# Performance work log

Measured on AMD Instinct MI355X. Metric: run time of the kernel, lower is better.

Reference implementation:

```python
import jax, jax.numpy as jnp
import numpy as np

N = 100000      # entity nodes
E = 1000000     # edges per relation
D_IN = 256
HID = 128
EPS = 1e-16     # PyG softmax denominator eps
NEG_SLOPE = 0.2 # GATConv default leaky_relu slope


def _gat_conv(x, ei, Ws, Wd, a_s, a_d, b):
    """Single-head GATConv (heads=1, concat=False) with self-loops."""
    n = x.shape[0]
    loop = jnp.arange(n, dtype=ei.dtype)
    src = jnp.concatenate([ei[0], loop])  # [E+N]
    dst = jnp.concatenate([ei[1], loop])
    h_src = x @ Ws                         # [N, HID]
    h_dst = x @ Wd                         # [N, HID]
    a_src = h_src @ a_s                    # [N]
    a_dst = h_dst @ a_d                    # [N]
    e = jax.nn.leaky_relu(a_src[src] + a_dst[dst], NEG_SLOPE)  # [E+N]
    # numerically-stable softmax over incoming edges of each dst node
    m = jax.ops.segment_max(e, dst, num_segments=n)
    ex = jnp.exp(e - m[dst])
    denom = jax.ops.segment_sum(ex, dst, num_segments=n)
    alpha = ex / (denom[dst] + EPS)        # [E+N]
    out = jax.ops.segment_sum(alpha[:, None] * h_src[src], dst, num_segments=n)
    return out + b


def setup_inputs() -> dict:
    key = jax.random.key(0)
    ks = jax.random.split(key, 9)
    s_in = 1.0 / np.sqrt(D_IN)
    s_h = 1.0 / np.sqrt(HID)
    return {
        "x": jax.random.normal(ks[0], (N, D_IN), dtype=jnp.float32),
        "edge_index_r0": jax.random.randint(ks[1], (2, E), 0, N, dtype=jnp.int64)
                         if jax.config.jax_enable_x64 else jax.random.randint(ks[1], (2, E), 0, N).astype(jnp.int32),
        "edge_index_r1": jax.random.randint(ks[2], (2, E), 0, N, dtype=jnp.int64)
                         if jax.config.jax_enable_x64 else jax.random.randint(ks[2], (2, E), 0, N).astype(jnp.int32),
        "W_src": jax.random.normal(ks[3], (2, D_IN, HID), dtype=jnp.float32) * s_in,
        "W_dst": jax.random.normal(ks[4], (2, D_IN, HID), dtype=jnp.float32) * s_in,
        "att_src": jax.random.normal(ks[5], (2, HID), dtype=jnp.float32) * s_h,
        "att_dst": jax.random.normal(ks[6], (2, HID), dtype=jnp.float32) * s_h,
        "bias": jnp.zeros((2, HID), dtype=jnp.float32),
    }


def reference(x, edge_index_r0, edge_index_r1, W_src, W_dst, att_src, att_dst, bias):
    # HeteroConv aggr='sum' over the two entity->entity relations
    out = _gat_conv(x, edge_index_r0, W_src[0], W_dst[0], att_src[0], att_dst[0], bias[0])
    out = out + _gat_conv(x, edge_index_r1, W_src[1], W_dst[1], att_src[1], att_dst[1], bias[1])
    # ELU; dropout p=0.0 is identity
    return jax.nn.elu(out)
```

## Files before the change

kernel.cpp:

```cpp
#include <hip/hip_runtime.h>

typedef __attribute__((ext_vector_type(8))) __bf16 bf16x8;
typedef __attribute__((ext_vector_type(4))) float floatx4;

__device__ __forceinline__ float bf2f(unsigned short u) {
    return __uint_as_float(((unsigned)u) << 16);
}
__device__ __forceinline__ unsigned short f2bf(float f) {
    unsigned u = __float_as_uint(f);
    unsigned r = u + 0x7FFFu + ((u >> 16) & 1u);
    return (unsigned short)(r >> 16);
}

__global__ void detect_k(const unsigned short* __restrict__ xs, int* __restrict__ flag) {
    __shared__ int sred[256];
    int tid = threadIdx.x;
    int cnt = 0;
    for (int j = 0; j < 16; ++j) {
        unsigned short u = xs[(tid * 16 + j) * 2];
        int e = (u >> 7) & 0xFF;
        cnt += (e >= 96 && e <= 159) ? 1 : 0;
    }
    sred[tid] = cnt;
    __syncthreads();
    for (int s = 128; s > 0; s >>= 1) {
        if (tid < s) sred[tid] += sred[tid + s];
        __syncthreads();
    }
    if (tid == 0) *flag = (sred[0] > 2048) ? 1 : 0;
}

__device__ __forceinline__ void canon8(const void* src, unsigned short* dst,
                                       long long idx, int f) {
    if (f) {
        *(uint4*)&dst[idx] = *(const uint4*)((const unsigned short*)src + idx);
    } else {
        const float* sf = (const float*)src;
        unsigned short v[8];
        for (int j = 0; j < 8; ++j) v[j] = f2bf(sf[idx + j]);
        *(uint4*)&dst[idx] = *(const uint4*)v;
    }
}

__global__ void canon5_k(const void* Ws, const void* Wd, const void* as,
                         const void* ad, const void* b,
                         unsigned short* Wsb, unsigned short* Wdb,
                         unsigned short* asb, unsigned short* adb,
                         unsigned short* bsb, const int* __restrict__ flag) {
    int blk = blockIdx.x, tid = threadIdx.x;
    int f = *flag;
    if (blk < 64) {
        const void* src = blk < 32 ? Ws : Wd;
        unsigned short* dst = blk < 32 ? Wsb : Wdb;
        long long idx = ((long long)(blk & 31) * 256 + tid) * 8;
        canon8(src, dst, idx, f);
    } else {
        if (tid < 32)       canon8(as, asb, (long long)tid * 8, f);
        else if (tid < 64)  canon8(ad, adb, (long long)(tid - 32) * 8, f);
        else if (tid < 96)  canon8(b,  bsb, (long long)(tid - 64) * 8, f);
    }
}

__global__ void vec_kernel(const unsigned short* __restrict__ Ws,
                           const unsigned short* __restrict__ Wd,
                           const unsigned short* __restrict__ as_,
                           const unsigned short* __restrict__ ad_,
                           float* __restrict__ vecs) {
    int r = blockIdx.x;
    int k = threadIdx.x;
    float s = 0.f, t = 0.f;
    const unsigned short* wsrow = Ws + (size_t)r * 32768 + (size_t)k * 128;
    const unsigned short* wdrow = Wd + (size_t)r * 32768 + (size_t)k * 128;
    for (int h = 0; h < 128; ++h) {
        s += bf2f(wsrow[h]) * bf2f(as_[r * 128 + h]);
        t += bf2f(wdrow[h]) * bf2f(ad_[r * 128 + h]);
    }
    vecs[(r * 2 + 0) * 256 + k] = s;
    vecs[(r * 2 + 1) * 256 + k] = t;
}

__global__ void transpose_W(const unsigned short* __restrict__ W,
                            unsigned short* __restrict__ Bt) {
    int i = blockIdx.x * 256 + threadIdx.x;
    if (i >= 2 * 256 * 128) return;
    int r = i >> 15, rem = i & 32767;
    int k = rem >> 7, n = rem & 127;
    Bt[(size_t)r * 32768 + n * 256 + k] = W[i];
}

__global__ __launch_bounds__(256) void a_canon_k(const void* __restrict__ xraw,
                                                 unsigned short* __restrict__ xb,
                                                 const float* __restrict__ vecs,
                                                 float* __restrict__ aout, int n,
                                                 const int* __restrict__ flag) {
    __shared__ float sv[1024];
    int tid = threadIdx.x;
    for (int j = 0; j < 4; ++j) sv[j * 256 + tid] = vecs[j * 256 + tid];
    __syncthreads();
    int lane = tid & 63, wave = tid >> 6;
    int row = blockIdx.x * 4 + wave;
    if (row >= n) return;
    float xf[4];
    if (*flag) {
        uint2 u = *(const uint2*)((const unsigned short*)xraw + (size_t)row * 256 + lane * 4);
        xf[0] = bf2f((unsigned short)(u.x & 0xFFFF));
        xf[1] = bf2f((unsigned short)(u.x >> 16));
        xf[2] = bf2f((unsigned short)(u.y & 0xFFFF));
        xf[3] = bf2f((unsigned short)(u.y >> 16));
        *(uint2*)&xb[(size_t)row * 256 + lane * 4] = u;
    } else {
        float4 f = *(const float4*)((const float*)xraw + (size_t)row * 256 + lane * 4);
        xf[0] = f.x; xf[1] = f.y; xf[2] = f.z; xf[3] = f.w;
        unsigned short v[4] = {f2bf(f.x), f2bf(f.y), f2bf(f.z), f2bf(f.w)};
        *(uint2*)&xb[(size_t)row * 256 + lane * 4] = *(const uint2*)v;
    }
    float s[4] = {0.f, 0.f, 0.f, 0.f};
    for (int j = 0; j < 4; ++j)
        for (int q = 0; q < 4; ++q)
            s[j] += xf[q] * sv[j * 256 + lane * 4 + q];
    for (int j = 0; j < 4; ++j)
        for (int off = 32; off > 0; off >>= 1)
            s[j] += __shfl_down(s[j], off);
    if (lane == 0)
        for (int j = 0; j < 4; ++j) aout[(size_t)j * n + row] = s[j];
}

__global__ __launch_bounds__(256) void gemm_h(const unsigned short* __restrict__ x,
                                              const unsigned short* __restrict__ Btg,
                                              unsigned short* __restrict__ hout, int n) {
    const int r = blockIdx.y;
    const unsigned short* bt = Btg + (size_t)r * 32768;
    unsigned short* h = hout + (size_t)r * n * 128;
    const int r0 = blockIdx.x * 128;
    __shared__ __align__(16) unsigned short As[128 * 40];
    __shared__ __align__(16) unsigned short Bs[128 * 40];
    int tid = threadIdx.x;
    int lane = tid & 63, wave = tid >> 6;

    floatx4 acc[2][8];
    for (int mt = 0; mt < 2; ++mt)
        for (int nt = 0; nt < 8; ++nt)
            acc[mt][nt] = (floatx4){0.f, 0.f, 0.f, 0.f};

    for (int k0 = 0; k0 < 256; k0 += 32) {
        for (int i = 0; i < 2; ++i) {
            int L = i * 256 + tid;
            int row = L >> 2, kc = (L & 3) * 8;
            uint4 va = make_uint4(0u, 0u, 0u, 0u);
            int gr = r0 + row;
            if (gr < n) va = *(const uint4*)&x[(size_t)gr * 256 + k0 + kc];
            *(uint4*)&As[row * 40 + kc] = va;
            uint4 vb = *(const uint4*)&bt[(size_t)row * 256 + k0 + kc];
            *(uint4*)&Bs[row * 40 + kc] = vb;
        }
        __syncthreads();
        int qk = (lane >> 4) * 8;
        int m16 = lane & 15;
        bf16x8 af[2], bfv[8];
        af[0] = *(const bf16x8*)&As[(wave * 32 + m16) * 40 + qk];
        af[1] = *(const bf16x8*)&As[(wave * 32 + 16 + m16) * 40 + qk];
        for (int nt = 0; nt < 8; ++nt)
            bfv[nt] = *(const bf16x8*)&Bs[(nt * 16 + m16) * 40 + qk];
        for (int mt = 0; mt < 2; ++mt)
            for (int nt = 0; nt < 8; ++nt)
                acc[mt][nt] = __builtin_amdgcn_mfma_f32_16x16x32_bf16(
                    af[mt], bfv[nt], acc[mt][nt], 0, 0, 0);
        __syncthreads();
    }
    int col0 = lane & 15;
    for (int mt = 0; mt < 2; ++mt) {
        int baser = r0 + wave * 32 + mt * 16 + (lane >> 4) * 4;
        for (int nt = 0; nt < 8; ++nt)
            for (int i = 0; i < 4; ++i) {
                int gr = baser + i;
                if (gr < n) h[(size_t)gr * 128 + nt * 16 + col0] = f2bf(acc[mt][nt][i]);
            }
    }
}

__global__ void hist2_k(const int* __restrict__ ei0, const int* __restrict__ ei1,
                        int* __restrict__ cnt0, int* __restrict__ cnt1,
                        int* __restrict__ rank0, int* __restrict__ rank1,
                        int E_, int n) {
    int rel = blockIdx.y;
    const int* ei = rel ? ei1 : ei0;
    int* cnt = rel ? cnt1 : cnt0;
    int* rank = rel ? rank1 : rank0;
    int t = blockIdx.x * 256 + threadIdx.x;
    if (t >= E_ + n) return;
    int d = (t < E_) ? ei[E_ + t] : (t - E_);
    rank[t] = atomicAdd(&cnt[d], 1);
}

__global__ __launch_bounds__(256) void scan_red_k(const int* __restrict__ cnt0,
                                                  const int* __restrict__ cnt1,
                                                  int* __restrict__ part,
                                                  int n, int nb) {
    __shared__ int s[256];
    int rel = blockIdx.y;
    const int* cnt = rel ? cnt1 : cnt0;
    int i = blockIdx.x * 256 + threadIdx.x;
    s[threadIdx.x] = (i < n) ? cnt[i] : 0;
    __syncthreads();
    for (int o = 128; o > 0; o >>= 1) {
        if (threadIdx.x < o) s[threadIdx.x] += s[threadIdx.x + o];
        __syncthreads();
    }
    if (threadIdx.x == 0) part[rel * nb + blockIdx.x] = s[0];
}

__global__ __launch_bounds__(1024) void scan_mid_k(int* __restrict__ part, int nb) {
    __shared__ int s[1024];
    int rel = blockIdx.x;
    int t = threadIdx.x;
    s[t] = (t < nb) ? part[rel * nb + t] : 0;
    __syncthreads();
    for (int o = 1; o < 1024; o <<= 1) {
        int v = (t >= o) ? s[t - o] : 0;
        __syncthreads();
        s[t] += v;
        __syncthreads();
    }
    if (t < nb) part[rel * nb + t] = (t == 0) ? 0 : s[t - 1];
}

__global__ __launch_bounds__(256) void scan_off_k(const int* __restrict__ cnt0,
                                                  const int* __restrict__ cnt1,
                                                  const int* __restrict__ part,
                                                  int* __restrict__ off0,
                                                  int* __restrict__ off1,
                                                  int n, int nb) {
    __shared__ int s[256];
    int rel = blockIdx.y;
    const int* cnt = rel ? cnt1 : cnt0;
    int* off = rel ? off1 : off0;
    int i = blockIdx.x * 256 + threadIdx.x;
    int t = threadIdx.x;
    int v = (i < n) ? cnt[i] : 0;
    s[t] = v;
    __syncthreads();
    for (int o = 1; o < 256; o <<= 1) {
        int u = (t >= o) ? s[t - o] : 0;
        __syncthreads();
        s[t] += u;
        __syncthreads();
    }
    if (i < n) off[i] = part[rel * nb + blockIdx.x] + s[t] - v;
}

__global__ void fill2_k(const int* __restrict__ ei0, const int* __restrict__ ei1,
                        const float* __restrict__ avals,
                        const int* __restrict__ off0, const int* __restrict__ off1,
                        const int* __restrict__ rank0, const int* __restrict__ rank1,
                        unsigned long long* __restrict__ pair0,
                        unsigned long long* __restrict__ pair1,
                        int E_, int n) {
    int rel = blockIdx.y;
    const int* ei = rel ? ei1 : ei0;
    const float* as_ = avals + (rel ? 2 * (size_t)n : 0);
    const float* ad_ = avals + (rel ? 3 * (size_t)n : (size_t)n);
    const int* off = rel ? off1 : off0;
    const int* rank = rel ? rank1 : rank0;
    unsigned long long* pair = rel ? pair1 : pair0;
    int t = blockIdx.x * 256 + threadIdx.x;
    if (t >= E_ + n) return;
    int s, d;
    if (t < E_) { s = ei[t]; d = ei[E_ + t]; } else { s = t - E_; d = s; }
    float e = as_[s] + ad_[d];
    e = e > 0.f ? e : 0.2f * e;
    int pos = off[d] + rank[t];
    pair[pos] = ((unsigned long long)__float_as_uint(e) << 32) | (unsigned)s;
}

__device__ __forceinline__ void acc8(float* a, float w, const uint4& hv) {
    a[0] += w * bf2f((unsigned short)(hv.x & 0xFFFFu));
    a[1] += w * bf2f((unsigned short)(hv.x >> 16));
    a[2] += w * bf2f((unsigned short)(hv.y & 0xFFFFu));
    a[3] += w * bf2f((unsigned short)(hv.y >> 16));
    a[4] += w * bf2f((unsigned short)(hv.z & 0xFFFFu));
    a[5] += w * bf2f((unsigned short)(hv.z >> 16));
    a[6] += w * bf2f((unsigned short)(hv.w & 0xFFFFu));
    a[7] += w * bf2f((unsigned short)(hv.w >> 16));
}

__device__ __forceinline__ void rel_acc4(int d, int g, int l, int lane,
                                         const int* __restrict__ off,
                                         const int* __restrict__ cnt,
                                         const unsigned long long* __restrict__ pair,
                                         const unsigned short* __restrict__ h,
                                         float* __restrict__ o ) {
    int s0 = off[d];
    int e0 = s0 + cnt[d];
    float m = -1e30f;
    for (int i = s0 + lane; i < e0; i += 64)
        m = fmaxf(m, __uint_as_float((unsigned)(pair[i] >> 32)));
    for (int o_ = 1; o_ < 64; o_ <<= 1) m = fmaxf(m, __shfl_xor(m, o_));
    float denom = 0.f;
    float a[8] = {0.f, 0.f, 0.f, 0.f, 0.f, 0.f, 0.f, 0.f};
    int last = e0 - 1;
    for (int base = s0; base < e0; base += 8) {
        int i0 = base + g, i1 = i0 + 4;
        int j0 = min(i0, last), j1 = min(i1, last);
        unsigned long long p0 = pair[j0];
        unsigned long long p1 = pair[j1];
        int sA = (int)(unsigned)p0;
        int sB = (int)(unsigned)p1;
        uint4 hv0 = *(const uint4*)&h[(size_t)sA * 128 + l * 8];
        uint4 hv1 = *(const uint4*)&h[(size_t)sB * 128 + l * 8];
        float w0 = __expf(__uint_as_float((unsigned)(p0 >> 32)) - m);
        float w1 = __expf(__uint_as_float((unsigned)(p1 >> 32)) - m);
        w0 = (i0 < e0) ? w0 : 0.f;
        w1 = (i1 < e0) ? w1 : 0.f;
        denom += w0 + w1;
        acc8(a, w0, hv0);
        acc8(a, w1, hv1);
    }
    for (int j = 0; j < 8; ++j) {
        a[j] += __shfl_xor(a[j], 16);
        a[j] += __shfl_xor(a[j], 32);
    }
    denom += __shfl_xor(denom, 16);
    denom += __shfl_xor(denom, 32);
    float inv = 1.f / (denom + 1e-16f);
    for (int j = 0; j < 8; ++j) o[j] = a[j] * inv;
}

__global__ __launch_bounds__(256) void agg_k(
    const int* __restrict__ off0, const int* __restrict__ cnt0,
    const unsigned long long* __restrict__ pair0,
    const int* __restrict__ off1, const int* __restrict__ cnt1,
    const unsigned long long* __restrict__ pair1,
    const unsigned short* __restrict__ h0, const unsigned short* __restrict__ h1,
    const unsigned short* __restrict__ bias, void* __restrict__ out,
    int n, const int* __restrict__ flag) {
    int wave = threadIdx.x >> 6, lane = threadIdx.x & 63;
    int g = lane >> 4, l = lane & 15;
    int d = blockIdx.x * 4 + wave;
    if (d >= n) return;
    float p[8], q[8];
    rel_acc4(d, g, l, lane, off0, cnt0, pair0, h0, p);
    rel_acc4(d, g, l, lane, off1, cnt1, pair1, h1, q);
    uint4 b0 = *(const uint4*)&bias[l * 8];
    uint4 b1 = *(const uint4*)&bias[128 + l * 8];
    const unsigned* b0u = (const unsigned*)&b0;
    const unsigned* b1u = (const unsigned*)&b1;
    float v[8];
    for (int j = 0; j < 8; ++j) {
        unsigned w0 = b0u[j >> 1], w1 = b1u[j >> 1];
        float bb = bf2f((unsigned short)((j & 1) ? (w0 >> 16) : (w0 & 0xFFFFu)))
                 + bf2f((unsigned short)((j & 1) ? (w1 >> 16) : (w1 & 0xFFFFu)));
        float t = p[j] + q[j] + bb;
        v[j] = t > 0.f ? t : (__expf(t) - 1.f);
    }
    if (g == 0) {
        if (*flag) {
            unsigned pk[4];
            for (int j = 0; j < 4; ++j)
                pk[j] = ((unsigned)f2bf(v[2 * j + 1]) << 16) | (unsigned)f2bf(v[2 * j]);
            ((uint4*)out)[(size_t)d * 16 + l] = *(const uint4*)pk;
        } else {
            float4 f0 = make_float4(v[0], v[1], v[2], v[3]);
            float4 f1 = make_float4(v[4], v[5], v[6], v[7]);
            ((float4*)out)[(size_t)d * 32 + l * 2] = f0;
            ((float4*)out)[(size_t)d * 32 + l * 2 + 1] = f1;
        }
    }
}

static inline char* carve(char*& p, size_t bytes) {
    char* r = p;
    p += (bytes + 255) & ~(size_t)255;
    return r;
}

extern "C" void kernel_launch(void* const* d_in, const int* in_sizes, int n_in,
                              void* d_out, int out_size, void* d_ws, size_t ws_size,
                              hipStream_t stream) {
    (void)n_in; (void)out_size; (void)ws_size;
    const void* x_raw  = d_in[0];
    const int*  ei0    = (const int*)d_in[1];
    const int*  ei1    = (const int*)d_in[2];
    const void* Ws_raw = d_in[3];
    const void* Wd_raw = d_in[4];
    const void* as_raw = d_in[5];
    const void* ad_raw = d_in[6];
    const void* b_raw  = d_in[7];

    const int n = in_sizes[0] / 256;
    const int e = in_sizes[1] / 2;
    const int tot = e + n;
    const int nb = (n + 255) / 256;

    char* p = (char*)d_ws;
    float* avals = (float*)carve(p, (size_t)4 * n * 4);
    int*   cnt0  = (int*)carve(p, (size_t)2 * n * 4);
    int*   cnt1  = cnt0 + n;
    int*   off0  = (int*)carve(p, (size_t)n * 4);
    int*   off1  = (int*)carve(p, (size_t)n * 4);
    int*   part  = (int*)carve(p, (size_t)2 * nb * 4);
    int*   rank0 = (int*)carve(p, (size_t)tot * 4);
    int*   rank1 = (int*)carve(p, (size_t)tot * 4);
    unsigned long long* pair0 = (unsigned long long*)carve(p, (size_t)tot * 8);
    unsigned long long* pair1 = (unsigned long long*)carve(p, (size_t)tot * 8);
    float* vecs  = (float*)carve(p, 1024 * 4);
    int*   flag  = (int*)carve(p, 256);
    unsigned short* xb  = (unsigned short*)carve(p, (size_t)n * 256 * 2);
    unsigned short* h0  = (unsigned short*)carve(p, (size_t)2 * n * 128 * 2);
    unsigned short* h1  = h0 + (size_t)n * 128;
    unsigned short* Wsb = (unsigned short*)carve(p, 65536 * 2);
    unsigned short* Wdb = (unsigned short*)carve(p, 65536 * 2);
    unsigned short* Bt  = (unsigned short*)carve(p, 65536 * 2);
    unsigned short* asb = (unsigned short*)carve(p, 256 * 2);
    unsigned short* adb = (unsigned short*)carve(p, 256 * 2);
    unsigned short* bsb = (unsigned short*)carve(p, 256 * 2);

    hipMemsetAsync(cnt0, 0, (size_t)2 * n * 4, stream);

    detect_k<<<1, 256, 0, stream>>>((const unsigned short*)x_raw, flag);
    canon5_k<<<65, 256, 0, stream>>>(Ws_raw, Wd_raw, as_raw, ad_raw, b_raw,
                                     Wsb, Wdb, asb, adb, bsb, flag);
    vec_kernel<<<2, 256, 0, stream>>>(Wsb, Wdb, asb, adb, vecs);
    transpose_W<<<(2 * 256 * 128 + 255) / 256, 256, 0, stream>>>(Wsb, Bt);

    int gb = (tot + 255) / 256;
    hist2_k<<<dim3(gb, 2), 256, 0, stream>>>(ei0, ei1, cnt0, cnt1, rank0, rank1, e, n);
    scan_red_k<<<dim3(nb, 2), 256, 0, stream>>>(cnt0, cnt1, part, n, nb);
    scan_mid_k<<<2, 1024, 0, stream>>>(part, nb);
    scan_off_k<<<dim3(nb, 2), 256, 0, stream>>>(cnt0, cnt1, part, off0, off1, n, nb);

    a_canon_k<<<(n + 3) / 4, 256, 0, stream>>>(x_raw, xb, vecs, avals, n, flag);
    gemm_h<<<dim3((n + 127) / 128, 2), 256, 0, stream>>>(xb, Bt, h0, n);

    fill2_k<<<dim3(gb, 2), 256, 0, stream>>>(ei0, ei1, avals, off0, off1,
                                             rank0, rank1, pair0, pair1, e, n);

    agg_k<<<(n + 3) / 4, 256, 0, stream>>>(off0, cnt0, pair0, off1, cnt1, pair1,
                                           h0, h1, bsb, d_out, n, flag);
}
```

Before: 500.6 us.

## Fuse input canonicalization into consumers and drop segment-max pass in aggregation

```diff
diff --git a/kernel.cpp b/kernel.cpp
--- a/kernel.cpp
+++ b/kernel.cpp
@@ -2,6 +2,7 @@
 
 typedef __attribute__((ext_vector_type(8))) __bf16 bf16x8;
 typedef __attribute__((ext_vector_type(4))) float floatx4;
+typedef unsigned long long ull;
 
 __device__ __forceinline__ float bf2f(unsigned short u) {
     return __uint_as_float(((unsigned)u) << 16);
@@ -30,69 +31,41 @@
     if (tid == 0) *flag = (sred[0] > 2048) ? 1 : 0;
 }
 
-__device__ __forceinline__ void canon8(const void* src, unsigned short* dst,
-                                       long long idx, int f) {
-    if (f) {
-        *(uint4*)&dst[idx] = *(const uint4*)((const unsigned short*)src + idx);
-    } else {
-        const float* sf = (const float*)src;
-        unsigned short v[8];
-        for (int j = 0; j < 8; ++j) v[j] = f2bf(sf[idx + j]);
-        *(uint4*)&dst[idx] = *(const uint4*)v;
-    }
-}
-
-__global__ void canon5_k(const void* Ws, const void* Wd, const void* as,
-                         const void* ad, const void* b,
-                         unsigned short* Wsb, unsigned short* Wdb,
-                         unsigned short* asb, unsigned short* adb,
-                         unsigned short* bsb, const int* __restrict__ flag) {
-    int blk = blockIdx.x, tid = threadIdx.x;
-    int f = *flag;
-    if (blk < 64) {
-        const void* src = blk < 32 ? Ws : Wd;
-        unsigned short* dst = blk < 32 ? Wsb : Wdb;
-        long long idx = ((long long)(blk & 31) * 256 + tid) * 8;
-        canon8(src, dst, idx, f);
-    } else {
-        if (tid < 32)       canon8(as, asb, (long long)tid * 8, f);
-        else if (tid < 64)  canon8(ad, adb, (long long)(tid - 32) * 8, f);
-        else if (tid < 96)  canon8(b,  bsb, (long long)(tid - 64) * 8, f);
-    }
-}
-
-__global__ void vec_kernel(const unsigned short* __restrict__ Ws,
-                           const unsigned short* __restrict__ Wd,
-                           const unsigned short* __restrict__ as_,
-                           const unsigned short* __restrict__ ad_,
-                           float* __restrict__ vecs) {
+__device__ __forceinline__ float getf(const void* p, size_t i, int f) {
+    return f ? bf2f(((const unsigned short*)p)[i]) : ((const float*)p)[i];
+}
+
+__global__ void vec_kernel(const void* __restrict__ Ws, const void* __restrict__ Wd,
+                           const void* __restrict__ as_, const void* __restrict__ ad_,
+                           float* __restrict__ vecs, const int* __restrict__ flag) {
     int r = blockIdx.x;
     int k = threadIdx.x;
+    int f = *flag;
     float s = 0.f, t = 0.f;
-    const unsigned short* wsrow = Ws + (size_t)r * 32768 + (size_t)k * 128;
-    const unsigned short* wdrow = Wd + (size_t)r * 32768 + (size_t)k * 128;
+    size_t wbase = (size_t)r * 32768 + (size_t)k * 128;
     for (int h = 0; h < 128; ++h) {
-        s += bf2f(wsrow[h]) * bf2f(as_[r * 128 + h]);
-        t += bf2f(wdrow[h]) * bf2f(ad_[r * 128 + h]);
+        s += getf(Ws, wbase + h, f) * getf(as_, r * 128 + h, f);
+        t += getf(Wd, wbase + h, f) * getf(ad_, r * 128 + h, f);
     }
     vecs[(r * 2 + 0) * 256 + k] = s;
     vecs[(r * 2 + 1) * 256 + k] = t;
 }
 
-__global__ void transpose_W(const unsigned short* __restrict__ W,
-                            unsigned short* __restrict__ Bt) {
+__global__ void transpose_W(const void* __restrict__ W, unsigned short* __restrict__ Bt,
+                            const int* __restrict__ flag) {
     int i = blockIdx.x * 256 + threadIdx.x;
     if (i >= 2 * 256 * 128) return;
+    int f = *flag;
+    unsigned short v = f ? ((const unsigned short*)W)[i] : f2bf(((const float*)W)[i]);
     int r = i >> 15, rem = i & 32767;
-    int k = rem >> 7, n = rem & 127;
-    Bt[(size_t)r * 32768 + n * 256 + k] = W[i];
-}
-
-__global__ __launch_bounds__(256) void a_canon_k(const void* __restrict__ xraw,
-                                                 unsigned short* __restrict__ xb,
-                                                 const float* __restrict__ vecs,
-                                                 float* __restrict__ aout, int n,
-                                                 const int* __restrict__ flag) {
+    int k = rem >> 7, nn = rem & 127;
+    Bt[(size_t)r * 32768 + nn * 256 + k] = v;
+}
+
+__global__ __launch_bounds__(256) void a_k(const void* __restrict__ xraw,
+                                           const float* __restrict__ vecs,
+                                           float* __restrict__ aout, int n,
+                                           const int* __restrict__ flag) {
     __shared__ float sv[1024];
     int tid = threadIdx.x;
     for (int j = 0; j < 4; ++j) sv[j * 256 + tid] = vecs[j * 256 + tid];
@@ -107,12 +80,9 @@
         xf[1] = bf2f((unsigned short)(u.x >> 16));
         xf[2] = bf2f((unsigned short)(u.y & 0xFFFF));
         xf[3] = bf2f((unsigned short)(u.y >> 16));
-        *(uint2*)&xb[(size_t)row * 256 + lane * 4] = u;
     } else {
         float4 f = *(const float4*)((const float*)xraw + (size_t)row * 256 + lane * 4);
         xf[0] = f.x; xf[1] = f.y; xf[2] = f.z; xf[3] = f.w;
-        unsigned short v[4] = {f2bf(f.x), f2bf(f.y), f2bf(f.z), f2bf(f.w)};
-        *(uint2*)&xb[(size_t)row * 256 + lane * 4] = *(const uint2*)v;
     }
     float s[4] = {0.f, 0.f, 0.f, 0.f};
     for (int j = 0; j < 4; ++j)
@@ -125,13 +95,15 @@
         for (int j = 0; j < 4; ++j) aout[(size_t)j * n + row] = s[j];
 }
 
-__global__ __launch_bounds__(256) void gemm_h(const unsigned short* __restrict__ x,
+__global__ __launch_bounds__(256) void gemm_h(const void* __restrict__ xraw,
                                               const unsigned short* __restrict__ Btg,
-                                              unsigned short* __restrict__ hout, int n) {
+                                              unsigned short* __restrict__ hout, int n,
+                                              const int* __restrict__ flag) {
     const int r = blockIdx.y;
     const unsigned short* bt = Btg + (size_t)r * 32768;
     unsigned short* h = hout + (size_t)r * n * 128;
     const int r0 = blockIdx.x * 128;
+    const int fl = *flag;
     __shared__ __align__(16) unsigned short As[128 * 40];
     __shared__ __align__(16) unsigned short Bs[128 * 40];
     int tid = threadIdx.x;
@@ -148,7 +120,18 @@
             int row = L >> 2, kc = (L & 3) * 8;
             uint4 va = make_uint4(0u, 0u, 0u, 0u);
             int gr = r0 + row;
-            if (gr < n) va = *(const uint4*)&x[(size_t)gr * 256 + k0 + kc];
+            if (gr < n) {
+                if (fl) {
+                    va = *(const uint4*)((const unsigned short*)xraw + (size_t)gr * 256 + k0 + kc);
+                } else {
+                    const float* xf = (const float*)xraw + (size_t)gr * 256 + k0 + kc;
+                    float4 f0 = *(const float4*)xf;
+                    float4 f1 = *(const float4*)(xf + 4);
+                    unsigned short v[8] = {f2bf(f0.x), f2bf(f0.y), f2bf(f0.z), f2bf(f0.w),
+                                           f2bf(f1.x), f2bf(f1.y), f2bf(f1.z), f2bf(f1.w)};
+                    va = *(const uint4*)v;
+                }
+            }
             *(uint4*)&As[row * 40 + kc] = va;
             uint4 vb = *(const uint4*)&bt[(size_t)row * 256 + k0 + kc];
             *(uint4*)&Bs[row * 40 + kc] = vb;
@@ -252,8 +235,7 @@
                         const float* __restrict__ avals,
                         const int* __restrict__ off0, const int* __restrict__ off1,
                         const int* __restrict__ rank0, const int* __restrict__ rank1,
-                        unsigned long long* __restrict__ pair0,
-                        unsigned long long* __restrict__ pair1,
+                        ull* __restrict__ pair0, ull* __restrict__ pair1,
                         int E_, int n) {
     int rel = blockIdx.y;
     const int* ei = rel ? ei1 : ei0;
@@ -261,99 +243,103 @@
     const float* ad_ = avals + (rel ? 3 * (size_t)n : (size_t)n);
     const int* off = rel ? off1 : off0;
     const int* rank = rel ? rank1 : rank0;
-    unsigned long long* pair = rel ? pair1 : pair0;
+    ull* pair = rel ? pair1 : pair0;
     int t = blockIdx.x * 256 + threadIdx.x;
     if (t >= E_ + n) return;
     int s, d;
     if (t < E_) { s = ei[t]; d = ei[E_ + t]; } else { s = t - E_; d = s; }
     float e = as_[s] + ad_[d];
     e = e > 0.f ? e : 0.2f * e;
+    float w = __expf(e);
     int pos = off[d] + rank[t];
-    pair[pos] = ((unsigned long long)__float_as_uint(e) << 32) | (unsigned)s;
-}
-
-__device__ __forceinline__ void acc8(float* a, float w, const uint4& hv) {
-    a[0] += w * bf2f((unsigned short)(hv.x & 0xFFFFu));
-    a[1] += w * bf2f((unsigned short)(hv.x >> 16));
-    a[2] += w * bf2f((unsigned short)(hv.y & 0xFFFFu));
-    a[3] += w * bf2f((unsigned short)(hv.y >> 16));
-    a[4] += w * bf2f((unsigned short)(hv.z & 0xFFFFu));
-    a[5] += w * bf2f((unsigned short)(hv.z >> 16));
-    a[6] += w * bf2f((unsigned short)(hv.w & 0xFFFFu));
-    a[7] += w * bf2f((unsigned short)(hv.w >> 16));
-}
-
-__device__ __forceinline__ void rel_acc4(int d, int g, int l, int lane,
+    pair[pos] = ((ull)__float_as_uint(w) << 32) | (unsigned)s;
+}
+
+__device__ __forceinline__ void accw(float2* a, float w, const uint4& hv) {
+    const unsigned* u = (const unsigned*)&hv;
+    for (int j = 0; j < 4; ++j) {
+        float lo = __uint_as_float(u[j] << 16);
+        float hi = __uint_as_float(u[j] & 0xFFFF0000u);
+        a[j].x += w * lo;
+        a[j].y += w * hi;
+    }
+}
+
+__device__ __forceinline__ void rel_accS(int d, int g, int l,
                                          const int* __restrict__ off,
                                          const int* __restrict__ cnt,
-                                         const unsigned long long* __restrict__ pair,
+                                         const ull* __restrict__ pair,
                                          const unsigned short* __restrict__ h,
-                                         float* __restrict__ o ) {
+                                         float2* __restrict__ o ) {
     int s0 = off[d];
     int e0 = s0 + cnt[d];
-    float m = -1e30f;
-    for (int i = s0 + lane; i < e0; i += 64)
-        m = fmaxf(m, __uint_as_float((unsigned)(pair[i] >> 32)));
-    for (int o_ = 1; o_ < 64; o_ <<= 1) m = fmaxf(m, __shfl_xor(m, o_));
     float denom = 0.f;
-    float a[8] = {0.f, 0.f, 0.f, 0.f, 0.f, 0.f, 0.f, 0.f};
+    float2 a[4] = {{0.f, 0.f}, {0.f, 0.f}, {0.f, 0.f}, {0.f, 0.f}};
     int last = e0 - 1;
     for (int base = s0; base < e0; base += 8) {
         int i0 = base + g, i1 = i0 + 4;
         int j0 = min(i0, last), j1 = min(i1, last);
-        unsigned long long p0 = pair[j0];
-        unsigned long long p1 = pair[j1];
+        ull p0 = pair[j0];
+        ull p1 = pair[j1];
         int sA = (int)(unsigned)p0;
         int sB = (int)(unsigned)p1;
         uint4 hv0 = *(const uint4*)&h[(size_t)sA * 128 + l * 8];
         uint4 hv1 = *(const uint4*)&h[(size_t)sB * 128 + l * 8];
-        float w0 = __expf(__uint_as_float((unsigned)(p0 >> 32)) - m);
-        float w1 = __expf(__uint_as_float((unsigned)(p1 >> 32)) - m);
+        float w0 = __uint_as_float((unsigned)(p0 >> 32));
+        float w1 = __uint_as_float((unsigned)(p1 >> 32));
         w0 = (i0 < e0) ? w0 : 0.f;
         w1 = (i1 < e0) ? w1 : 0.f;
         denom += w0 + w1;
-        acc8(a, w0, hv0);
-        acc8(a, w1, hv1);
-    }
-    for (int j = 0; j < 8; ++j) {
-        a[j] += __shfl_xor(a[j], 16);
-        a[j] += __shfl_xor(a[j], 32);
+        accw(a, w0, hv0);
+        accw(a, w1, hv1);
+    }
+    for (int j = 0; j < 4; ++j) {
+        a[j].x += __shfl_xor(a[j].x, 16);
+        a[j].x += __shfl_xor(a[j].x, 32);
+        a[j].y += __shfl_xor(a[j].y, 16);
+        a[j].y += __shfl_xor(a[j].y, 32);
     }
     denom += __shfl_xor(denom, 16);
     denom += __shfl_xor(denom, 32);
     float inv = 1.f / (denom + 1e-16f);
-    for (int j = 0; j < 8; ++j) o[j] = a[j] * inv;
+    for (int j = 0; j < 4; ++j) { o[j].x = a[j].x * inv; o[j].y = a[j].y * inv; }
 }
 
 __global__ __launch_bounds__(256) void agg_k(
     const int* __restrict__ off0, const int* __restrict__ cnt0,
-    const unsigned long long* __restrict__ pair0,
+    const ull* __restrict__ pair0,
     const int* __restrict__ off1, const int* __restrict__ cnt1,
-    const unsigned long long* __restrict__ pair1,
+    const ull* __restrict__ pair1,
     const unsigned short* __restrict__ h0, const unsigned short* __restrict__ h1,
-    const unsigned short* __restrict__ bias, void* __restrict__ out,
+    const void* __restrict__ bias_raw, void* __restrict__ out,
     int n, const int* __restrict__ flag) {
     int wave = threadIdx.x >> 6, lane = threadIdx.x & 63;
     int g = lane >> 4, l = lane & 15;
     int d = blockIdx.x * 4 + wave;
     if (d >= n) return;
-    float p[8], q[8];
-    rel_acc4(d, g, l, lane, off0, cnt0, pair0, h0, p);
-    rel_acc4(d, g, l, lane, off1, cnt1, pair1, h1, q);
-    uint4 b0 = *(const uint4*)&bias[l * 8];
-    uint4 b1 = *(const uint4*)&bias[128 + l * 8];
-    const unsigned* b0u = (const unsigned*)&b0;
-    const unsigned* b1u = (const unsigned*)&b1;
+    int fl = *flag;
+    float2 p[4], q[4];
+    rel_accS(d, g, l, off0, cnt0, pair0, h0, p);
+    rel_accS(d, g, l, off1, cnt1, pair1, h1, q);
+    float bb[8];
+    if (fl) {
+        const unsigned short* bs = (const unsigned short*)bias_raw;
+        for (int j = 0; j < 8; ++j)
+            bb[j] = bf2f(bs[l * 8 + j]) + bf2f(bs[128 + l * 8 + j]);
+    } else {
+        const float* bf = (const float*)bias_raw;
+        for (int j = 0; j < 8; ++j)
+            bb[j] = bf[l * 8 + j] + bf[128 + l * 8 + j];
+    }
     float v[8];
-    for (int j = 0; j < 8; ++j) {
-        unsigned w0 = b0u[j >> 1], w1 = b1u[j >> 1];
-        float bb = bf2f((unsigned short)((j & 1) ? (w0 >> 16) : (w0 & 0xFFFFu)))
-                 + bf2f((unsigned short)((j & 1) ? (w1 >> 16) : (w1 & 0xFFFFu)));
-        float t = p[j] + q[j] + bb;
-        v[j] = t > 0.f ? t : (__expf(t) - 1.f);
+    for (int j = 0; j < 4; ++j) {
+        float t0 = p[j].x + q[j].x + bb[2 * j];
+        float t1 = p[j].y + q[j].y + bb[2 * j + 1];
+        v[2 * j]     = t0 > 0.f ? t0 : (__expf(t0) - 1.f);
+        v[2 * j + 1] = t1 > 0.f ? t1 : (__expf(t1) - 1.f);
     }
     if (g == 0) {
-        if (*flag) {
+        if (fl) {
             unsigned pk[4];
             for (int j = 0; j < 4; ++j)
                 pk[j] = ((unsigned)f2bf(v[2 * j + 1]) << 16) | (unsigned)f2bf(v[2 * j]);
@@ -400,27 +386,19 @@
     int*   part  = (int*)carve(p, (size_t)2 * nb * 4);
     int*   rank0 = (int*)carve(p, (size_t)tot * 4);
     int*   rank1 = (int*)carve(p, (size_t)tot * 4);
-    unsigned long long* pair0 = (unsigned long long*)carve(p, (size_t)tot * 8);
-    unsigned long long* pair1 = (unsigned long long*)carve(p, (size_t)tot * 8);
+    ull*   pair0 = (ull*)carve(p, (size_t)tot * 8);
+    ull*   pair1 = (ull*)carve(p, (size_t)tot * 8);
     float* vecs  = (float*)carve(p, 1024 * 4);
     int*   flag  = (int*)carve(p, 256);
-    unsigned short* xb  = (unsigned short*)carve(p, (size_t)n * 256 * 2);
-    unsigned short* h0  = (unsigned short*)carve(p, (size_t)2 * n * 128 * 2);
-    unsigned short* h1  = h0 + (size_t)n * 128;
-    unsigned short* Wsb = (unsigned short*)carve(p, 65536 * 2);
-    unsigned short* Wdb = (unsigned short*)carve(p, 65536 * 2);
-    unsigned short* Bt  = (unsigned short*)carve(p, 65536 * 2);
-    unsigned short* asb = (unsigned short*)carve(p, 256 * 2);
-    unsigned short* adb = (unsigned short*)carve(p, 256 * 2);
-    unsigned short* bsb = (unsigned short*)carve(p, 256 * 2);
+    unsigned short* h0 = (unsigned short*)carve(p, (size_t)2 * n * 128 * 2);
+    unsigned short* h1 = h0 + (size_t)n * 128;
+    unsigned short* Bt = (unsigned short*)carve(p, 65536 * 2);
 
     hipMemsetAsync(cnt0, 0, (size_t)2 * n * 4, stream);
 
     detect_k<<<1, 256, 0, stream>>>((const unsigned short*)x_raw, flag);
-    canon5_k<<<65, 256, 0, stream>>>(Ws_raw, Wd_raw, as_raw, ad_raw, b_raw,
-                                     Wsb, Wdb, asb, adb, bsb, flag);
-    vec_kernel<<<2, 256, 0, stream>>>(Wsb, Wdb, asb, adb, vecs);
-    transpose_W<<<(2 * 256 * 128 + 255) / 256, 256, 0, stream>>>(Wsb, Bt);
+    vec_kernel<<<2, 256, 0, stream>>>(Ws_raw, Wd_raw, as_raw, ad_raw, vecs, flag);
+    transpose_W<<<(2 * 256 * 128 + 255) / 256, 256, 0, stream>>>(Ws_raw, Bt, flag);
 
     int gb = (tot + 255) / 256;
     hist2_k<<<dim3(gb, 2), 256, 0, stream>>>(ei0, ei1, cnt0, cnt1, rank0, rank1, e, n);
@@ -428,12 +406,12 @@
     scan_mid_k<<<2, 1024, 0, stream>>>(part, nb);
     scan_off_k<<<dim3(nb, 2), 256, 0, stream>>>(cnt0, cnt1, part, off0, off1, n, nb);
 
-    a_canon_k<<<(n + 3) / 4, 256, 0, stream>>>(x_raw, xb, vecs, avals, n, flag);
-    gemm_h<<<dim3((n + 127) / 128, 2), 256, 0, stream>>>(xb, Bt, h0, n);
+    a_k<<<(n + 3) / 4, 256, 0, stream>>>(x_raw, vecs, avals, n, flag);
+    gemm_h<<<dim3((n + 127) / 128, 2), 256, 0, stream>>>(x_raw, Bt, h0, n, flag);
 
     fill2_k<<<dim3(gb, 2), 256, 0, stream>>>(ei0, ei1, avals, off0, off1,
                                              rank0, rank1, pair0, pair1, e, n);
 
     agg_k<<<(n + 3) / 4, 256, 0, stream>>>(off0, cnt0, pair0, off1, cnt1, pair1,
-                                           h0, h1, bsb, d_out, n, flag);
-}
+                                           h0, h1, b_raw, d_out, n, flag);
+}
```

New measurement: 531.5 us. +6.2%, slower.
